# Kernel optimization log

Hardware: AMD Instinct MI355X
Metric: run time of the kernel (lower is better)

The kernel has to match this reference:

```python
import jax, jax.numpy as jnp
import numpy as np
from jax import lax

T = 16384          # num_tokens
H = 512            # hidden_size
HC = 4             # hc_mult
NGRAM = 4          # max_ngram_size -> conv dilation
N_EMBED = 256      # n_embed_per_ngram
N_HEADPN = 4       # n_head_per_ngram
NUM_HEADS = (NGRAM - 1) * N_HEADPN          # 12 embedding heads
HEAD_DIM = N_EMBED // N_HEADPN              # 64
E = (NGRAM - 1) * N_EMBED                   # 768 = engram_hidden_size
VOCAB = 50000
K = 4              # conv kernel_size
EPS = 1e-5         # layernorm_eps
GATE_EPS = 1e-6


def setup_inputs() -> dict:
    key = jax.random.key(0)
    ks = jax.random.split(key, 8)
    hash_ids = jax.random.randint(ks[0], (T, NUM_HEADS), 0, VOCAB, dtype=jnp.int32)
    offsets = jnp.asarray(np.concatenate([[0], np.cumsum([VOCAB] * (NUM_HEADS - 1))]).astype(np.int32))
    embedding_weight = jax.random.normal(ks[1], (NUM_HEADS * VOCAB, HEAD_DIM), jnp.float32) * 0.02
    key_projs_w = jax.random.normal(ks[2], (HC, E, H), jnp.float32) * 0.02
    q_norm_w = jnp.ones((HC, H), jnp.float32)
    k_norm_w = jnp.ones((HC, H), jnp.float32)
    v_proj_w = jax.random.normal(ks[3], (E, H), jnp.float32) * 0.02
    conv_w = jax.random.normal(ks[4], (HC * H, K), jnp.float32) * 0.1
    conv_norm_w = jnp.ones((HC, H), jnp.float32)
    hidden_states = jax.random.normal(ks[5], (T, HC, H), jnp.float32)
    return {
        'hash_ids': hash_ids, 'offsets': offsets, 'embedding_weight': embedding_weight,
        'key_projs_w': key_projs_w, 'q_norm_w': q_norm_w, 'k_norm_w': k_norm_w,
        'v_proj_w': v_proj_w, 'conv_w': conv_w, 'conv_norm_w': conv_norm_w,
        'hidden_states': hidden_states,
    }


def _group_rms_norm(x, w, eps=EPS):
    # x: [G, T, H], w: [G, H]; RMS over last dim, per-group affine scale
    inv = lax.rsqrt(jnp.mean(x * x, axis=-1, keepdims=True) + eps)
    return x * inv * w[:, None, :]


def reference(hash_ids, offsets, embedding_weight, key_projs_w, q_norm_w, k_norm_w,
              v_proj_w, conv_w, conv_norm_w, hidden_states):
    num_tokens, hc_mult, hidden = hidden_states.shape
    # --- MultiHeadEmbedding: hash-indexed gather into a concatenated table ---
    emb = embedding_weight[hash_ids + offsets[None, :]]          # [T, NUM_HEADS, HEAD_DIM]
    emb = emb.reshape(num_tokens, E)                              # [T, E]
    # --- key projection per hc group (bmm) ---
    keys = jnp.einsum('te,geh->gth', emb, key_projs_w)            # [HC, T, H]
    key_n = _group_rms_norm(keys, k_norm_w)
    query_n = _group_rms_norm(hidden_states.transpose(1, 0, 2), q_norm_w)  # [HC, T, H]
    # --- scaled dot-product gate ---
    scale = 1.0 / jnp.sqrt(jnp.asarray(hidden, hidden_states.dtype))
    gate = jax.nn.sigmoid(jnp.sum(key_n * query_n, axis=-1) * scale)       # [HC, T]
    gate = gate.T[:, :, None]                                     # [T, HC, 1]
    # --- value projection + gating ---
    value = gate * (emb @ v_proj_w)[:, None, :]                   # [T, HC, H]
    # --- ShortConv: GroupRMSNorm + depthwise dilated causal conv1d + SiLU ---
    x_n = _group_rms_norm(value.transpose(1, 0, 2), conv_norm_w)  # [HC, T, H]
    x_bct = x_n.transpose(0, 2, 1).reshape(1, hc_mult * hidden, num_tokens)  # [1, C, T]
    pad = NGRAM * (K - 1)
    y = lax.conv_general_dilated(
        x_bct, conv_w[:, None, :],                                # kernel [C, 1, K]
        window_strides=(1,), padding=[(pad, 0)], rhs_dilation=(NGRAM,),
        feature_group_count=hc_mult * hidden,
        dimension_numbers=('NCH', 'OIH', 'NCH'))
    y = jax.nn.silu(y)[0]                                         # [C, T]
    y = y.reshape(hc_mult, hidden, num_tokens).transpose(2, 0, 1) # [T, HC, H]
    return value + y


if __name__ == '__main__':
    out = reference(**setup_inputs())
    print(out.shape, out.dtype)
```

## Files before the change

kernel.cpp:

```cpp
#include <hip/hip_runtime.h>
#include <hip/hip_bf16.h>
#include <math.h>

#define T_TOK  16384
#define H_DIM  512
#define NHEADS 12
#define E_DIM  768
#define EPS_N  1e-5f
#define QK_SCALE 0.04419417382415922f

typedef unsigned short u16;
typedef __bf16 bf16;
typedef bf16   bf16x8 __attribute__((ext_vector_type(8)));
typedef float  f32x4  __attribute__((ext_vector_type(4)));
typedef u16    u16x4  __attribute__((ext_vector_type(4)));
typedef u16    u16x8  __attribute__((ext_vector_type(8)));

__device__ __forceinline__ u16 f2bf(float f) {
  unsigned u = __builtin_bit_cast(unsigned, f);
  unsigned r = u + 0x7fffu + ((u >> 16) & 1u);
  return (u16)(r >> 16);
}
__device__ __forceinline__ float bf2f(u16 h) {
  unsigned u = ((unsigned)h) << 16;
  return __builtin_bit_cast(float, u);
}

__global__ __launch_bounds__(256) void gather_emb(
    const int* __restrict__ hash_ids, const int* __restrict__ offsets,
    const float* __restrict__ emb_w, u16* __restrict__ emb) {
  int idx = blockIdx.x * 256 + threadIdx.x;
  int pair = idx >> 3;
  int sub = idx & 7;
  int t = pair / 12;
  int head = pair - t * 12;
  int row = hash_ids[pair] + offsets[head];
  const float* src = emb_w + (size_t)row * 64 + sub * 8;
  float4 a = *(const float4*)src;
  float4 b = *(const float4*)(src + 4);
  u16x8 o;
  o[0] = f2bf(a.x); o[1] = f2bf(a.y); o[2] = f2bf(a.z); o[3] = f2bf(a.w);
  o[4] = f2bf(b.x); o[5] = f2bf(b.y); o[6] = f2bf(b.z); o[7] = f2bf(b.w);
  *(u16x8*)(emb + (size_t)t * E_DIM + head * 64 + sub * 8) = o;
}

__global__ __launch_bounds__(256) void build_wcat(
    const float* __restrict__ kp, const float* __restrict__ vp,
    u16* __restrict__ wt) {
  __shared__ float tile[32][33];
  int m = blockIdx.z;
  const float* src = (m < 4) ? (kp + (size_t)m * E_DIM * H_DIM) : vp;
  int h0 = blockIdx.x * 32, e0 = blockIdx.y * 32;
  int tx = threadIdx.x, ty = threadIdx.y;
  #pragma unroll
  for (int j = 0; j < 32; j += 8)
    tile[ty + j][tx] = src[(size_t)(e0 + ty + j) * H_DIM + h0 + tx];
  __syncthreads();
  #pragma unroll
  for (int j = 0; j < 32; j += 8) {
    int h = h0 + ty + j, e = e0 + tx;
    wt[(size_t)(m * H_DIM + h) * E_DIM + e] = f2bf(tile[tx][ty + j]);
  }
}

__global__ __launch_bounds__(256) void build_wc(
    const float* __restrict__ conv_w, const float* __restrict__ cnw,
    const float* __restrict__ qw, const float* __restrict__ kw,
    float* __restrict__ wc, float* __restrict__ qwkw) {
  int cf = blockIdx.x * 256 + threadIdx.x;
  float c = cnw[cf];
  #pragma unroll
  for (int k = 0; k < 4; ++k) wc[k * 2048 + cf] = conv_w[cf * 4 + k] * c;
  qwkw[cf] = qw[cf] * kw[cf];
}

__global__ __launch_bounds__(256, 2) void gemm_bf16(
    const u16* __restrict__ A, const u16* __restrict__ BT,
    const float* __restrict__ hidden, const float* __restrict__ qwkw,
    u16* __restrict__ V, float* __restrict__ kssP, float* __restrict__ qkP,
    float* __restrict__ qssP, float* __restrict__ msvP) {
  __shared__ __align__(16) char smem[50176];
  u16 (*As)[64] = (u16(*)[64])smem;
  u16 (*Bs)[64] = (u16(*)[64])(smem + 16384);
  u16*    qlds  = (u16*)smem;
  float2* red2h = (float2*)(smem + 33792);
  float*  red1  = (float*)smem;
  const int K = E_DIM;
  int tid = threadIdx.x;
  int lane = tid & 63, wid = tid >> 6;

  int orig = blockIdx.x + blockIdx.y * 20;
  int swz = (orig & 7) * 320 + (orig >> 3);
  int bx = swz % 20, by = swz / 20;

  int wm = (wid >> 1) * 64, wn = (wid & 1) * 64;
  int widN = wid & 1;
  int lr16 = lane & 15, rgrp = lane >> 4;

  const u16* aptr = A + (size_t)(by * 128 + (tid >> 3)) * K + (tid & 7) * 8;
  const u16* bptr = BT + (size_t)(bx * 128 + (tid >> 3)) * K + (tid & 7) * 8;
  int lds_off = tid * 16;

  f32x4 acc[4][4] = {};

  for (int k0 = 0; k0 < K; k0 += 64) {
    #pragma unroll
    for (int r = 0; r < 4; ++r) {
      __builtin_amdgcn_global_load_lds(
        (const __attribute__((address_space(1))) void*)(aptr + (size_t)(r * 32) * K + k0),
        (__attribute__((address_space(3))) void*)(smem + r * 4096 + lds_off),
        16, 0, 0);
      __builtin_amdgcn_global_load_lds(
        (const __attribute__((address_space(1))) void*)(bptr + (size_t)(r * 32) * K + k0),
        (__attribute__((address_space(3))) void*)(smem + 16384 + r * 4096 + lds_off),
        16, 0, 0);
    }
    __syncthreads();
    int lk8 = (lane >> 4) * 8;
    #pragma unroll
    for (int kk = 0; kk < 2; ++kk) {
      bf16x8 af[4], bfv[4];
      #pragma unroll
      for (int m = 0; m < 4; ++m)
        af[m] = *reinterpret_cast<const bf16x8*>(&As[wm + m * 16 + lr16][kk * 32 + lk8]);
      #pragma unroll
      for (int n = 0; n < 4; ++n)
        bfv[n] = *reinterpret_cast<const bf16x8*>(&Bs[wn + n * 16 + lr16][kk * 32 + lk8]);
      #pragma unroll
      for (int m = 0; m < 4; ++m)
        #pragma unroll
        for (int n = 0; n < 4; ++n)
          acc[m][n] = __builtin_amdgcn_mfma_f32_16x16x32_bf16(af[m], bfv[n], acc[m][n], 0, 0, 0);
    }
    __syncthreads();
  }

  if (bx < 16) {
    int g = bx >> 2, qq = bx & 3;
    const float* hq = hidden + (size_t)(by * 128) * 2048 + g * 512 + qq * 128;
    float s2[8];
    #pragma unroll
    for (int p = 0; p < 8; ++p) {
      int row = p * 16 + (tid >> 4);
      int col = (tid & 15) * 8;
      const float* src = hq + (size_t)row * 2048 + col;
      float4 x0 = *(const float4*)src;
      float4 x1 = *(const float4*)(src + 4);
      float qv[8] = {x0.x, x0.y, x0.z, x0.w, x1.x, x1.y, x1.z, x1.w};
      u16x8 o;
      float ss = 0.f;
      #pragma unroll
      for (int j = 0; j < 8; ++j) { ss += qv[j] * qv[j]; o[j] = f2bf(qv[j]); }
      s2[p] = ss;
      *(u16x8*)&qlds[row * 132 + col] = o;
    }
    #pragma unroll
    for (int off = 1; off < 16; off <<= 1)
      #pragma unroll
      for (int p = 0; p < 8; ++p) s2[p] += __shfl_xor(s2[p], off, 64);
    if ((tid & 15) == 0) {
      #pragma unroll
      for (int p = 0; p < 8; ++p) {
        int t = by * 128 + p * 16 + (tid >> 4);
        qssP[(t * 4 + g) * 4 + qq] = s2[p];
      }
    }
    __syncthreads();

    int colg = g * 512 + qq * 128 + wn + lr16;
    float w4[4];
    #pragma unroll
    for (int n = 0; n < 4; ++n) w4[n] = qwkw[colg + n * 16];
    #pragma unroll
    for (int m = 0; m < 4; ++m) {
      #pragma unroll
      for (int j = 0; j < 4; ++j) {
        int r = wm + m * 16 + rgrp * 4 + j;
        float sk2 = 0.f, sqk = 0.f;
        #pragma unroll
        for (int n = 0; n < 4; ++n) {
          float kv = acc[m][n][j];
          float qv = bf2f(qlds[r * 132 + wn + n * 16 + lr16]);
          sk2 += kv * kv;
          sqk += qv * w4[n] * kv;
        }
        sk2 += __shfl_xor(sk2, 8, 64);
        sqk += __shfl_xor(sqk, 8, 64);
        if (lr16 < 8) red2h[(widN * 128 + r) * 8 + lr16] = make_float2(sk2, sqk);
      }
    }
    __syncthreads();
    if (tid < 128) {
      float s0 = 0.f, s1 = 0.f;
      #pragma unroll
      for (int j = 0; j < 8; ++j) {
        int jj = (j + tid) & 7;
        float2 a = red2h[tid * 8 + jj];
        float2 b = red2h[(128 + tid) * 8 + jj];
        s0 += a.x + b.x;
        s1 += a.y + b.y;
      }
      int t = by * 128 + tid;
      int o = (t * 4 + g) * 4 + qq;
      kssP[o] = s0;
      qkP[o]  = s1;
    }
  } else {
    int q2i = bx - 16;
    #pragma unroll
    for (int m = 0; m < 4; ++m) {
      #pragma unroll
      for (int j = 0; j < 4; ++j) {
        int r = wm + m * 16 + rgrp * 4 + j;
        size_t t = (size_t)(by * 128 + r);
        float sv2 = 0.f;
        #pragma unroll
        for (int n = 0; n < 4; ++n) {
          float v = acc[m][n][j];
          sv2 += v * v;
          V[t * 512 + q2i * 128 + wn + n * 16 + lr16] = f2bf(v);
        }
        red1[(widN * 128 + r) * 16 + lr16] = sv2;
      }
    }
    __syncthreads();
    if (tid < 128) {
      float s = 0.f;
      #pragma unroll
      for (int j = 0; j < 16; ++j) {
        int jj = (j + tid) & 15;
        s += red1[tid * 16 + jj] + red1[(128 + tid) * 16 + jj];
      }
      int t = by * 128 + tid;
      msvP[t * 4 + q2i] = s;
    }
  }
}

__global__ __launch_bounds__(256) void gate_finish(
    const float* __restrict__ kssP, const float* __restrict__ qkP,
    const float* __restrict__ qssP, const float* __restrict__ msvP,
    float* __restrict__ gateA, float* __restrict__ aA) {
  int i = blockIdx.x * 256 + threadIdx.x;
  int t = i >> 2;
  float4 k4 = *(const float4*)&kssP[i * 4];
  float4 d4 = *(const float4*)&qkP[i * 4];
  float4 q4 = *(const float4*)&qssP[i * 4];
  float4 m4 = *(const float4*)&msvP[t * 4];
  float kss = k4.x + k4.y + k4.z + k4.w;
  float qk  = d4.x + d4.y + d4.z + d4.w;
  float qss = q4.x + q4.y + q4.z + q4.w;
  float msv = (m4.x + m4.y + m4.z + m4.w) * (1.0f / 512.0f);
  float qinv = rsqrtf(qss * (1.0f / 512.0f) + EPS_N);
  float kinv = rsqrtf(kss * (1.0f / 512.0f) + EPS_N);
  float gate = 1.0f / (1.0f + __expf(-qk * qinv * kinv * QK_SCALE));
  gateA[i] = gate;
  aA[i] = gate * rsqrtf(gate * gate * msv + EPS_N);
}

__global__ __launch_bounds__(256) void out_kernel(
    const u16* __restrict__ V,
    const float* __restrict__ gateA, const float* __restrict__ aA,
    const float* __restrict__ wc,
    float* __restrict__ out) {
  int idx = blockIdx.x * 256 + threadIdx.x;
  int t = idx >> 8;
  int c8 = (idx & 255) * 8;
  int g = c8 >> 9;
  int h = c8 & 511;

  float acc[8] = {0.f, 0.f, 0.f, 0.f, 0.f, 0.f, 0.f, 0.f};
  float vr_t[8];
  #pragma unroll
  for (int k = 0; k < 4; ++k) {
    int tk = t - 12 + 4 * k;
    if (tk < 0) continue;
    float s = aA[tk * 4 + g];
    u16x8 vv = *(const u16x8*)&V[(size_t)tk * 512 + h];
    float4 w0 = *(const float4*)(wc + k * 2048 + c8);
    float4 w1 = *(const float4*)(wc + k * 2048 + c8 + 4);
    float w8[8] = {w0.x, w0.y, w0.z, w0.w, w1.x, w1.y, w1.z, w1.w};
    #pragma unroll
    for (int j = 0; j < 8; ++j) {
      float v = bf2f(vv[j]);
      acc[j] += w8[j] * s * v;
      if (k == 3) vr_t[j] = v;
    }
  }
  float gate = gateA[t * 4 + g];
  float r[8];
  #pragma unroll
  for (int j = 0; j < 8; ++j) {
    float y = acc[j];
    r[j] = gate * vr_t[j] + y / (1.0f + __expf(-y));
  }
  float* op = out + (size_t)t * 2048 + c8;
  *(float4*)op       = make_float4(r[0], r[1], r[2], r[3]);
  *(float4*)(op + 4) = make_float4(r[4], r[5], r[6], r[7]);
}

extern "C" void kernel_launch(void* const* d_in, const int* in_sizes, int n_in,
                              void* d_out, int out_size, void* d_ws, size_t ws_size,
                              hipStream_t stream) {
  const int*   hash_ids = (const int*)d_in[0];
  const int*   offsets  = (const int*)d_in[1];
  const float* emb_w    = (const float*)d_in[2];
  const float* kp       = (const float*)d_in[3];
  const float* qw       = (const float*)d_in[4];
  const float* kw       = (const float*)d_in[5];
  const float* vp       = (const float*)d_in[6];
  const float* conv_w   = (const float*)d_in[7];
  const float* cw       = (const float*)d_in[8];
  const float* hidden   = (const float*)d_in[9];
  float* out = (float*)d_out;
  char*  ws  = (char*)d_ws;

  u16*   V     = (u16*)ws;
  u16*   emb   = (u16*)(ws + 16777216);
  u16*   wt    = (u16*)(ws + 41943040);
  float* kssP  = (float*)(ws + 45875200);
  float* qkP   = (float*)(ws + 46923776);
  float* qssP  = (float*)(ws + 47972352);
  float* msvP  = (float*)(ws + 49020928);
  float* gateA = (float*)(ws + 49283072);
  float* aA    = (float*)(ws + 49545216);
  float* wc    = (float*)(ws + 49807360);
  float* qwkw  = (float*)(ws + 49840128);

  gather_emb<<<(T_TOK * 12 * 8) / 256, 256, 0, stream>>>(hash_ids, offsets, emb_w, emb);
  build_wcat<<<dim3(16, 24, 5), dim3(32, 8), 0, stream>>>(kp, vp, wt);
  build_wc<<<8, 256, 0, stream>>>(conv_w, cw, qw, kw, wc, qwkw);
  gemm_bf16<<<dim3(20, 128), 256, 0, stream>>>(emb, wt, hidden, qwkw,
                                               V, kssP, qkP, qssP, msvP);
  gate_finish<<<(T_TOK * 4) / 256, 256, 0, stream>>>(kssP, qkP, qssP, msvP, gateA, aA);
  out_kernel<<<T_TOK * 256 / 256, 256, 0, stream>>>(V, gateA, aA, wc, out);
}
```

Before: 184.0 us.

## Rewrite GEMM with 256x256 tiles, double-buffered LDS and XOR swizzle

The fused bf16 GEMM moves from 128x128 tiles with 256 threads to 256x256 tiles with 512 threads and 128 KB of LDS. Global-to-LDS loads are double-buffered with explicit vmcnt waits, LDS addresses are XOR-swizzled to avoid bank conflicts, and MFMA blocks run at raised priority. The goal is more data reuse per tile and overlap of loads with compute. The cost is occupancy of one block per CU, a more complex epilogue that loops over two 128-column query chunks, and a 2-way partial for the value sum of squares.

```diff
diff --git a/kernel.cpp b/kernel.cpp
--- a/kernel.cpp
+++ b/kernel.cpp
@@ -3,8 +3,6 @@
 #include <math.h>
 
 #define T_TOK  16384
-#define H_DIM  512
-#define NHEADS 12
 #define E_DIM  768
 #define EPS_N  1e-5f
 #define QK_SCALE 0.04419417382415922f
@@ -49,17 +47,17 @@
     u16* __restrict__ wt) {
   __shared__ float tile[32][33];
   int m = blockIdx.z;
-  const float* src = (m < 4) ? (kp + (size_t)m * E_DIM * H_DIM) : vp;
+  const float* src = (m < 4) ? (kp + (size_t)m * E_DIM * 512) : vp;
   int h0 = blockIdx.x * 32, e0 = blockIdx.y * 32;
   int tx = threadIdx.x, ty = threadIdx.y;
   #pragma unroll
   for (int j = 0; j < 32; j += 8)
-    tile[ty + j][tx] = src[(size_t)(e0 + ty + j) * H_DIM + h0 + tx];
+    tile[ty + j][tx] = src[(size_t)(e0 + ty + j) * 512 + h0 + tx];
   __syncthreads();
   #pragma unroll
   for (int j = 0; j < 32; j += 8) {
     int h = h0 + ty + j, e = e0 + tx;
-    wt[(size_t)(m * H_DIM + h) * E_DIM + e] = f2bf(tile[tx][ty + j]);
+    wt[(size_t)(m * 512 + h) * E_DIM + e] = f2bf(tile[tx][ty + j]);
   }
 }
 
@@ -74,167 +72,185 @@
   qwkw[cf] = qw[cf] * kw[cf];
 }
 
-__global__ __launch_bounds__(256, 2) void gemm_bf16(
+__global__ __launch_bounds__(512, 1) void gemm_bf16(
     const u16* __restrict__ A, const u16* __restrict__ BT,
     const float* __restrict__ hidden, const float* __restrict__ qwkw,
     u16* __restrict__ V, float* __restrict__ kssP, float* __restrict__ qkP,
     float* __restrict__ qssP, float* __restrict__ msvP) {
-  __shared__ __align__(16) char smem[50176];
-  u16 (*As)[64] = (u16(*)[64])smem;
-  u16 (*Bs)[64] = (u16(*)[64])(smem + 16384);
-  u16*    qlds  = (u16*)smem;
-  float2* red2h = (float2*)(smem + 33792);
-  float*  red1  = (float*)smem;
+  __shared__ __align__(16) char smem[131072];
   const int K = E_DIM;
   int tid = threadIdx.x;
   int lane = tid & 63, wid = tid >> 6;
-
-  int orig = blockIdx.x + blockIdx.y * 20;
-  int swz = (orig & 7) * 320 + (orig >> 3);
-  int bx = swz % 20, by = swz / 20;
-
-  int wm = (wid >> 1) * 64, wn = (wid & 1) * 64;
-  int widN = wid & 1;
+  int wr = wid >> 2, wc4 = wid & 3;
   int lr16 = lane & 15, rgrp = lane >> 4;
 
-  const u16* aptr = A + (size_t)(by * 128 + (tid >> 3)) * K + (tid & 7) * 8;
-  const u16* bptr = BT + (size_t)(bx * 128 + (tid >> 3)) * K + (tid & 7) * 8;
-  int lds_off = tid * 16;
-
-  f32x4 acc[4][4] = {};
-
-  for (int k0 = 0; k0 < K; k0 += 64) {
-    #pragma unroll
-    for (int r = 0; r < 4; ++r) {
-      __builtin_amdgcn_global_load_lds(
-        (const __attribute__((address_space(1))) void*)(aptr + (size_t)(r * 32) * K + k0),
-        (__attribute__((address_space(3))) void*)(smem + r * 4096 + lds_off),
-        16, 0, 0);
-      __builtin_amdgcn_global_load_lds(
-        (const __attribute__((address_space(1))) void*)(bptr + (size_t)(r * 32) * K + k0),
-        (__attribute__((address_space(3))) void*)(smem + 16384 + r * 4096 + lds_off),
-        16, 0, 0);
-    }
-    __syncthreads();
-    int lk8 = (lane >> 4) * 8;
+  int orig = blockIdx.x;
+  int swz = (orig & 7) * 80 + (orig >> 3);
+  int bx = swz % 10, by = swz / 10;
+
+  int srow = tid >> 3;
+  int sunit = ((tid & 7) ^ (srow & 7)) * 8;
+  const u16* aptr = A + (size_t)(by * 256 + srow) * K + sunit;
+  const u16* bptr = BT + (size_t)(bx * 256 + srow) * K + sunit;
+  int dst = tid * 16;
+
+  f32x4 acc[8][4] = {};
+
+#define STAGE(step, buf) { \
+    int k0 = (step) * 64; \
+    for (int r = 0; r < 4; ++r) \
+      __builtin_amdgcn_global_load_lds( \
+        (const __attribute__((address_space(1))) void*)(aptr + (size_t)(r * 64) * K + k0), \
+        (__attribute__((address_space(3))) void*)(smem + (buf) * 65536 + r * 8192 + dst), 16, 0, 0); \
+    for (int r = 0; r < 4; ++r) \
+      __builtin_amdgcn_global_load_lds( \
+        (const __attribute__((address_space(1))) void*)(bptr + (size_t)(r * 64) * K + k0), \
+        (__attribute__((address_space(3))) void*)(smem + (buf) * 65536 + 32768 + r * 8192 + dst), 16, 0, 0); \
+  }
+
+  STAGE(0, 0)
+  STAGE(1, 1)
+  asm volatile("s_waitcnt vmcnt(8)" ::: "memory");
+  __builtin_amdgcn_sched_barrier(0);
+  __builtin_amdgcn_s_barrier();
+  __builtin_amdgcn_sched_barrier(0);
+
+  int aoff = (wr * 128 + lr16) * 64;
+  int boff = (wc4 * 64 + lr16) * 64;
+  int swz8 = lr16 & 7;
+
+  for (int t = 0; t < 12; ++t) {
+    int cur = t & 1;
+    const u16* Ab = (const u16*)(smem + cur * 65536);
+    const u16* Bb = (const u16*)(smem + cur * 65536 + 32768);
     #pragma unroll
     for (int kk = 0; kk < 2; ++kk) {
-      bf16x8 af[4], bfv[4];
-      #pragma unroll
-      for (int m = 0; m < 4; ++m)
-        af[m] = *reinterpret_cast<const bf16x8*>(&As[wm + m * 16 + lr16][kk * 32 + lk8]);
+      int un = ((kk * 4 + rgrp) ^ swz8) * 8;
+      bf16x8 af[8], bfr[4];
+      #pragma unroll
+      for (int m = 0; m < 8; ++m)
+        af[m] = *(const bf16x8*)&Ab[aoff + m * 1024 + un];
       #pragma unroll
       for (int n = 0; n < 4; ++n)
-        bfv[n] = *reinterpret_cast<const bf16x8*>(&Bs[wn + n * 16 + lr16][kk * 32 + lk8]);
-      #pragma unroll
-      for (int m = 0; m < 4; ++m)
+        bfr[n] = *(const bf16x8*)&Bb[boff + n * 1024 + un];
+      __builtin_amdgcn_s_setprio(1);
+      #pragma unroll
+      for (int m = 0; m < 8; ++m)
         #pragma unroll
         for (int n = 0; n < 4; ++n)
-          acc[m][n] = __builtin_amdgcn_mfma_f32_16x16x32_bf16(af[m], bfv[n], acc[m][n], 0, 0, 0);
-    }
-    __syncthreads();
-  }
-
-  if (bx < 16) {
-    int g = bx >> 2, qq = bx & 3;
-    const float* hq = hidden + (size_t)(by * 128) * 2048 + g * 512 + qq * 128;
-    float s2[8];
+          acc[m][n] = __builtin_amdgcn_mfma_f32_16x16x32_bf16(af[m], bfr[n], acc[m][n], 0, 0, 0);
+      __builtin_amdgcn_s_setprio(0);
+    }
+    __builtin_amdgcn_sched_barrier(0);
+    __builtin_amdgcn_s_barrier();
+    __builtin_amdgcn_sched_barrier(0);
+    if (t + 2 < 12) STAGE(t + 2, cur)
+    __builtin_amdgcn_sched_barrier(0);
+    if (t <= 9)       { asm volatile("s_waitcnt vmcnt(8)" ::: "memory"); }
+    else if (t == 10) { asm volatile("s_waitcnt vmcnt(0)" ::: "memory"); }
+    __builtin_amdgcn_sched_barrier(0);
+    __builtin_amdgcn_s_barrier();
+    __builtin_amdgcn_sched_barrier(0);
+  }
+
+  u16*    hlds = (u16*)smem;
+  float2* red2 = (float2*)(smem + 98304);
+  float*  red1 = (float*)smem;
+
+  if (bx < 8) {
+    int g = bx >> 1, half = bx & 1;
+    #pragma unroll 1
+    for (int qloc = 0; qloc < 2; ++qloc) {
+      const float* hq = hidden + (size_t)(by * 256) * 2048 + g * 512 + half * 256 + qloc * 128;
+      int unit = tid & 31, rb = tid >> 5;
+      #pragma unroll 1
+      for (int rr = 0; rr < 16; ++rr) {
+        int row = rr * 16 + rb;
+        float4 x = *(const float4*)(hq + (size_t)row * 2048 + unit * 4);
+        float s = x.x * x.x + x.y * x.y + x.z * x.z + x.w * x.w;
+        u16x4 o; o[0] = f2bf(x.x); o[1] = f2bf(x.y); o[2] = f2bf(x.z); o[3] = f2bf(x.w);
+        *(u16x4*)&hlds[row * 130 + unit * 4] = o;
+        #pragma unroll
+        for (int mm = 1; mm < 32; mm <<= 1) s += __shfl_xor(s, mm, 64);
+        if ((lane & 31) == 0)
+          qssP[((by * 256 + row) * 4 + g) * 4 + half * 2 + qloc] = s;
+      }
+      __syncthreads();
+      if ((wc4 >> 1) == qloc) {
+        int wcL = wc4 & 1;
+        float w4[4];
+        #pragma unroll
+        for (int n = 0; n < 4; ++n)
+          w4[n] = qwkw[g * 512 + half * 256 + qloc * 128 + wcL * 64 + n * 16 + lr16];
+        #pragma unroll
+        for (int m = 0; m < 8; ++m) {
+          #pragma unroll
+          for (int j = 0; j < 4; ++j) {
+            int r = wr * 128 + m * 16 + rgrp * 4 + j;
+            float sk2 = 0.f, sqk = 0.f;
+            #pragma unroll
+            for (int n = 0; n < 4; ++n) {
+              float kv = acc[m][n][j];
+              float qv = bf2f(hlds[r * 130 + wcL * 64 + n * 16 + lr16]);
+              sk2 += kv * kv;
+              sqk += qv * w4[n] * kv;
+            }
+            sk2 += __shfl_xor(sk2, 8, 64);
+            sqk += __shfl_xor(sqk, 8, 64);
+            if (lr16 < 8) red2[(wcL * 256 + r) * 8 + lr16] = make_float2(sk2, sqk);
+          }
+        }
+      }
+      __syncthreads();
+      if (tid < 256) {
+        float s0 = 0.f, s1 = 0.f;
+        #pragma unroll
+        for (int j = 0; j < 8; ++j) {
+          int jj = (j + tid) & 7;
+          float2 a = red2[tid * 8 + jj];
+          float2 b = red2[(256 + tid) * 8 + jj];
+          s0 += a.x + b.x;
+          s1 += a.y + b.y;
+        }
+        int o = ((by * 256 + tid) * 4 + g) * 4 + half * 2 + qloc;
+        kssP[o] = s0;
+        qkP[o]  = s1;
+      }
+      __syncthreads();
+    }
+  } else {
+    int q2i = bx - 8;
     #pragma unroll
-    for (int p = 0; p < 8; ++p) {
-      int row = p * 16 + (tid >> 4);
-      int col = (tid & 15) * 8;
-      const float* src = hq + (size_t)row * 2048 + col;
-      float4 x0 = *(const float4*)src;
-      float4 x1 = *(const float4*)(src + 4);
-      float qv[8] = {x0.x, x0.y, x0.z, x0.w, x1.x, x1.y, x1.z, x1.w};
-      u16x8 o;
-      float ss = 0.f;
-      #pragma unroll
-      for (int j = 0; j < 8; ++j) { ss += qv[j] * qv[j]; o[j] = f2bf(qv[j]); }
-      s2[p] = ss;
-      *(u16x8*)&qlds[row * 132 + col] = o;
-    }
-    #pragma unroll
-    for (int off = 1; off < 16; off <<= 1)
-      #pragma unroll
-      for (int p = 0; p < 8; ++p) s2[p] += __shfl_xor(s2[p], off, 64);
-    if ((tid & 15) == 0) {
-      #pragma unroll
-      for (int p = 0; p < 8; ++p) {
-        int t = by * 128 + p * 16 + (tid >> 4);
-        qssP[(t * 4 + g) * 4 + qq] = s2[p];
-      }
-    }
-    __syncthreads();
-
-    int colg = g * 512 + qq * 128 + wn + lr16;
-    float w4[4];
-    #pragma unroll
-    for (int n = 0; n < 4; ++n) w4[n] = qwkw[colg + n * 16];
-    #pragma unroll
-    for (int m = 0; m < 4; ++m) {
+    for (int m = 0; m < 8; ++m) {
       #pragma unroll
       for (int j = 0; j < 4; ++j) {
-        int r = wm + m * 16 + rgrp * 4 + j;
-        float sk2 = 0.f, sqk = 0.f;
-        #pragma unroll
-        for (int n = 0; n < 4; ++n) {
-          float kv = acc[m][n][j];
-          float qv = bf2f(qlds[r * 132 + wn + n * 16 + lr16]);
-          sk2 += kv * kv;
-          sqk += qv * w4[n] * kv;
-        }
-        sk2 += __shfl_xor(sk2, 8, 64);
-        sqk += __shfl_xor(sqk, 8, 64);
-        if (lr16 < 8) red2h[(widN * 128 + r) * 8 + lr16] = make_float2(sk2, sqk);
-      }
-    }
-    __syncthreads();
-    if (tid < 128) {
-      float s0 = 0.f, s1 = 0.f;
-      #pragma unroll
-      for (int j = 0; j < 8; ++j) {
-        int jj = (j + tid) & 7;
-        float2 a = red2h[tid * 8 + jj];
-        float2 b = red2h[(128 + tid) * 8 + jj];
-        s0 += a.x + b.x;
-        s1 += a.y + b.y;
-      }
-      int t = by * 128 + tid;
-      int o = (t * 4 + g) * 4 + qq;
-      kssP[o] = s0;
-      qkP[o]  = s1;
-    }
-  } else {
-    int q2i = bx - 16;
-    #pragma unroll
-    for (int m = 0; m < 4; ++m) {
-      #pragma unroll
-      for (int j = 0; j < 4; ++j) {
-        int r = wm + m * 16 + rgrp * 4 + j;
-        size_t t = (size_t)(by * 128 + r);
+        int r = wr * 128 + m * 16 + rgrp * 4 + j;
+        size_t tg = (size_t)(by * 256 + r);
         float sv2 = 0.f;
         #pragma unroll
         for (int n = 0; n < 4; ++n) {
           float v = acc[m][n][j];
           sv2 += v * v;
-          V[t * 512 + q2i * 128 + wn + n * 16 + lr16] = f2bf(v);
+          V[tg * 512 + q2i * 256 + wc4 * 64 + n * 16 + lr16] = f2bf(v);
         }
-        red1[(widN * 128 + r) * 16 + lr16] = sv2;
+        sv2 += __shfl_xor(sv2, 8, 64);
+        if (lr16 < 8) red1[(wc4 * 256 + r) * 8 + lr16] = sv2;
       }
     }
     __syncthreads();
-    if (tid < 128) {
+    if (tid < 256) {
       float s = 0.f;
       #pragma unroll
-      for (int j = 0; j < 16; ++j) {
-        int jj = (j + tid) & 15;
-        s += red1[tid * 16 + jj] + red1[(128 + tid) * 16 + jj];
-      }
-      int t = by * 128 + tid;
-      msvP[t * 4 + q2i] = s;
-    }
-  }
+      for (int w = 0; w < 4; ++w)
+        #pragma unroll
+        for (int j = 0; j < 8; ++j) {
+          int jj = (j + tid) & 7;
+          s += red1[(w * 256 + tid) * 8 + jj];
+        }
+      msvP[(by * 256 + tid) * 2 + q2i] = s;
+    }
+  }
+#undef STAGE
 }
 
 __global__ __launch_bounds__(256) void gate_finish(
@@ -246,11 +262,11 @@
   float4 k4 = *(const float4*)&kssP[i * 4];
   float4 d4 = *(const float4*)&qkP[i * 4];
   float4 q4 = *(const float4*)&qssP[i * 4];
-  float4 m4 = *(const float4*)&msvP[t * 4];
+  float2 m2 = *(const float2*)&msvP[t * 2];
   float kss = k4.x + k4.y + k4.z + k4.w;
   float qk  = d4.x + d4.y + d4.z + d4.w;
   float qss = q4.x + q4.y + q4.z + q4.w;
-  float msv = (m4.x + m4.y + m4.z + m4.w) * (1.0f / 512.0f);
+  float msv = (m2.x + m2.y) * (1.0f / 512.0f);
   float qinv = rsqrtf(qss * (1.0f / 512.0f) + EPS_N);
   float kinv = rsqrtf(kss * (1.0f / 512.0f) + EPS_N);
   float gate = 1.0f / (1.0f + __expf(-qk * qinv * kinv * QK_SCALE));
@@ -330,8 +346,8 @@
   gather_emb<<<(T_TOK * 12 * 8) / 256, 256, 0, stream>>>(hash_ids, offsets, emb_w, emb);
   build_wcat<<<dim3(16, 24, 5), dim3(32, 8), 0, stream>>>(kp, vp, wt);
   build_wc<<<8, 256, 0, stream>>>(conv_w, cw, qw, kw, wc, qwkw);
-  gemm_bf16<<<dim3(20, 128), 256, 0, stream>>>(emb, wt, hidden, qwkw,
-                                               V, kssP, qkP, qssP, msvP);
+  gemm_bf16<<<640, 512, 0, stream>>>(emb, wt, hidden, qwkw,
+                                     V, kssP, qkP, qssP, msvP);
   gate_finish<<<(T_TOK * 4) / 256, 256, 0, stream>>>(kssP, qkP, qssP, msvP, gateA, aA);
   out_kernel<<<T_TOK * 256 / 256, 256, 0, stream>>>(V, gateA, aA, wc, out);
 }
```

Result: slower. 266.4 us (+44.8%).

## Shrink GEMM LDS footprint and XOR-swizzle tile layout to avoid bank conflicts

Applied to the files above, without the earlier changes.

Reduces the GEMM kernel's shared memory from about 49KB to 32KB by staging the hidden-state query tile in two 64-column halves, each consumed only by the matching wave column. It also XOR-swizzles the 16-byte units of the A/B LDS tiles so MFMA fragment reads avoid bank conflicts. The smaller LDS use is meant to allow more resident blocks per CU. The cost is an extra barrier pair in the epilogue, with half the waves idle during each phase.

```diff
diff --git a/kernel.cpp b/kernel.cpp
--- a/kernel.cpp
+++ b/kernel.cpp
@@ -79,12 +79,9 @@
     const float* __restrict__ hidden, const float* __restrict__ qwkw,
     u16* __restrict__ V, float* __restrict__ kssP, float* __restrict__ qkP,
     float* __restrict__ qssP, float* __restrict__ msvP) {
-  __shared__ __align__(16) char smem[50176];
+  __shared__ __align__(16) char smem[32768];
   u16 (*As)[64] = (u16(*)[64])smem;
   u16 (*Bs)[64] = (u16(*)[64])(smem + 16384);
-  u16*    qlds  = (u16*)smem;
-  float2* red2h = (float2*)(smem + 33792);
-  float*  red1  = (float*)smem;
   const int K = E_DIM;
   int tid = threadIdx.x;
   int lane = tid & 63, wid = tid >> 6;
@@ -96,9 +93,12 @@
   int wm = (wid >> 1) * 64, wn = (wid & 1) * 64;
   int widN = wid & 1;
   int lr16 = lane & 15, rgrp = lane >> 4;
-
-  const u16* aptr = A + (size_t)(by * 128 + (tid >> 3)) * K + (tid & 7) * 8;
-  const u16* bptr = BT + (size_t)(bx * 128 + (tid >> 3)) * K + (tid & 7) * 8;
+  int swz8 = lr16 & 7;
+
+  int srow = tid >> 3;
+  int sunit = ((tid & 7) ^ (srow & 7)) * 8;
+  const u16* aptr = A + (size_t)(by * 128 + srow) * K + sunit;
+  const u16* bptr = BT + (size_t)(bx * 128 + srow) * K + sunit;
   int lds_off = tid * 16;
 
   f32x4 acc[4][4] = {};
@@ -116,16 +116,16 @@
         16, 0, 0);
     }
     __syncthreads();
-    int lk8 = (lane >> 4) * 8;
     #pragma unroll
     for (int kk = 0; kk < 2; ++kk) {
+      int un = ((kk * 4 + rgrp) ^ swz8) * 8;
       bf16x8 af[4], bfv[4];
       #pragma unroll
       for (int m = 0; m < 4; ++m)
-        af[m] = *reinterpret_cast<const bf16x8*>(&As[wm + m * 16 + lr16][kk * 32 + lk8]);
+        af[m] = *reinterpret_cast<const bf16x8*>(&As[wm + m * 16 + lr16][un]);
       #pragma unroll
       for (int n = 0; n < 4; ++n)
-        bfv[n] = *reinterpret_cast<const bf16x8*>(&Bs[wn + n * 16 + lr16][kk * 32 + lk8]);
+        bfv[n] = *reinterpret_cast<const bf16x8*>(&Bs[wn + n * 16 + lr16][un]);
       #pragma unroll
       for (int m = 0; m < 4; ++m)
         #pragma unroll
@@ -137,75 +137,77 @@
 
   if (bx < 16) {
     int g = bx >> 2, qq = bx & 3;
-    const float* hq = hidden + (size_t)(by * 128) * 2048 + g * 512 + qq * 128;
-    float s2[8];
-    #pragma unroll
-    for (int p = 0; p < 8; ++p) {
-      int row = p * 16 + (tid >> 4);
-      int col = (tid & 15) * 8;
-      const float* src = hq + (size_t)row * 2048 + col;
-      float4 x0 = *(const float4*)src;
-      float4 x1 = *(const float4*)(src + 4);
-      float qv[8] = {x0.x, x0.y, x0.z, x0.w, x1.x, x1.y, x1.z, x1.w};
-      u16x8 o;
-      float ss = 0.f;
-      #pragma unroll
-      for (int j = 0; j < 8; ++j) { ss += qv[j] * qv[j]; o[j] = f2bf(qv[j]); }
-      s2[p] = ss;
-      *(u16x8*)&qlds[row * 132 + col] = o;
+    u16*    hlds = (u16*)smem;
+    float2* red2 = (float2*)(smem + 20480);
+    float s2[8] = {0.f, 0.f, 0.f, 0.f, 0.f, 0.f, 0.f, 0.f};
+    #pragma unroll 1
+    for (int hh = 0; hh < 2; ++hh) {
+      const float* hq = hidden + (size_t)(by * 128) * 2048 + g * 512 + qq * 128 + hh * 64;
+      #pragma unroll
+      for (int p = 0; p < 8; ++p) {
+        int row = p * 16 + (tid >> 4);
+        int c4 = (tid & 15) * 4;
+        float4 x = *(const float4*)(hq + (size_t)row * 2048 + c4);
+        s2[p] += x.x * x.x + x.y * x.y + x.z * x.z + x.w * x.w;
+        u16x4 o; o[0] = f2bf(x.x); o[1] = f2bf(x.y); o[2] = f2bf(x.z); o[3] = f2bf(x.w);
+        *(u16x4*)&hlds[row * 66 + c4] = o;
+      }
+      __syncthreads();
+      if (widN == hh) {
+        float w4[4];
+        #pragma unroll
+        for (int n = 0; n < 4; ++n)
+          w4[n] = qwkw[g * 512 + qq * 128 + hh * 64 + n * 16 + lr16];
+        #pragma unroll
+        for (int m = 0; m < 4; ++m) {
+          #pragma unroll
+          for (int j = 0; j < 4; ++j) {
+            int r = wm + m * 16 + rgrp * 4 + j;
+            float sk2 = 0.f, sqk = 0.f;
+            #pragma unroll
+            for (int n = 0; n < 4; ++n) {
+              float kv = acc[m][n][j];
+              float qv = bf2f(hlds[r * 66 + n * 16 + lr16]);
+              sk2 += kv * kv;
+              sqk += qv * w4[n] * kv;
+            }
+            sk2 += __shfl_xor(sk2, 8, 64);
+            sqk += __shfl_xor(sqk, 8, 64);
+            sk2 += __shfl_xor(sk2, 4, 64);
+            sqk += __shfl_xor(sqk, 4, 64);
+            if (lr16 < 4) red2[(hh * 128 + r) * 4 + lr16] = make_float2(sk2, sqk);
+          }
+        }
+      }
+      __syncthreads();
     }
     #pragma unroll
     for (int off = 1; off < 16; off <<= 1)
       #pragma unroll
       for (int p = 0; p < 8; ++p) s2[p] += __shfl_xor(s2[p], off, 64);
-    if ((tid & 15) == 0) {
+    if ((lane & 15) == 0) {
       #pragma unroll
       for (int p = 0; p < 8; ++p) {
-        int t = by * 128 + p * 16 + (tid >> 4);
-        qssP[(t * 4 + g) * 4 + qq] = s2[p];
-      }
-    }
-    __syncthreads();
-
-    int colg = g * 512 + qq * 128 + wn + lr16;
-    float w4[4];
-    #pragma unroll
-    for (int n = 0; n < 4; ++n) w4[n] = qwkw[colg + n * 16];
-    #pragma unroll
-    for (int m = 0; m < 4; ++m) {
-      #pragma unroll
-      for (int j = 0; j < 4; ++j) {
-        int r = wm + m * 16 + rgrp * 4 + j;
-        float sk2 = 0.f, sqk = 0.f;
-        #pragma unroll
-        for (int n = 0; n < 4; ++n) {
-          float kv = acc[m][n][j];
-          float qv = bf2f(qlds[r * 132 + wn + n * 16 + lr16]);
-          sk2 += kv * kv;
-          sqk += qv * w4[n] * kv;
-        }
-        sk2 += __shfl_xor(sk2, 8, 64);
-        sqk += __shfl_xor(sqk, 8, 64);
-        if (lr16 < 8) red2h[(widN * 128 + r) * 8 + lr16] = make_float2(sk2, sqk);
-      }
-    }
-    __syncthreads();
+        int trow = by * 128 + p * 16 + (tid >> 4);
+        qssP[(trow * 4 + g) * 4 + qq] = s2[p];
+      }
+    }
     if (tid < 128) {
       float s0 = 0.f, s1 = 0.f;
       #pragma unroll
-      for (int j = 0; j < 8; ++j) {
-        int jj = (j + tid) & 7;
-        float2 a = red2h[tid * 8 + jj];
-        float2 b = red2h[(128 + tid) * 8 + jj];
+      for (int j = 0; j < 4; ++j) {
+        int jj = (j + tid) & 3;
+        float2 a = red2[tid * 4 + jj];
+        float2 b = red2[(128 + tid) * 4 + jj];
         s0 += a.x + b.x;
         s1 += a.y + b.y;
       }
-      int t = by * 128 + tid;
-      int o = (t * 4 + g) * 4 + qq;
+      int o = ((by * 128 + tid) * 4 + g) * 4 + qq;
       kssP[o] = s0;
       qkP[o]  = s1;
     }
   } else {
+    float* red1 = (float*)smem;
     int q2i = bx - 16;
     #pragma unroll
     for (int m = 0; m < 4; ++m) {
```

Measured after the change: 222.1 us. 20.7% more time.
